# Optimization experiments

Hardware: AMD Instinct MI355X
Metric: run time of the kernel (lower is better)

## Reference

```python
import jax, jax.numpy as jnp
import numpy as np

EPS = 1e-12  # F.normalize default eps


def setup_inputs() -> dict:
    key = jax.random.key(0)
    k1, k2, k3, k4 = jax.random.split(key, 4)
    dim, heads = 192, 6
    B, H, W = 8, 128, 128
    x = jax.random.normal(k1, (B, dim, H, W), dtype=jnp.float32)
    qkv_w = jax.random.normal(k2, (3 * dim, dim), dtype=jnp.float32) * 0.05
    qkv_dw_w = jax.random.normal(k3, (3 * dim, 1, 3, 3), dtype=jnp.float32) * 0.05
    proj_w = jax.random.normal(k4, (dim, dim), dtype=jnp.float32) * 0.05
    temperature = jnp.ones((heads, 1, 1), dtype=jnp.float32)
    return {"x": x, "qkv_w": qkv_w, "qkv_dw_w": qkv_dw_w,
            "proj_w": proj_w, "temperature": temperature}


def _l2norm(t):
    # F.normalize(t, dim=-1): t / max(||t||_2, eps)
    n = jnp.sqrt(jnp.sum(t * t, axis=-1, keepdims=True))
    return t / jnp.maximum(n, EPS)


def reference(x, qkv_w, qkv_dw_w, proj_w, temperature):
    B, C, H, W = x.shape
    heads = temperature.shape[0]
    ch = C // heads  # channels per head

    # 1x1 pointwise conv (no bias)
    qkv = jnp.einsum('oc,bchw->bohw', qkv_w, x)
    # depthwise 3x3 conv, padding=1, groups = 3*C
    qkv = jax.lax.conv_general_dilated(
        qkv, qkv_dw_w, window_strides=(1, 1), padding='SAME',
        feature_group_count=3 * C,
        dimension_numbers=('NCHW', 'OIHW', 'NCHW'))

    q, k, v = jnp.split(qkv, 3, axis=1)
    # b (hd c) h w -> b hd c (h w)
    def split_heads(t):
        return t.reshape(B, heads, ch, H * W)
    q, k, v = split_heads(q), split_heads(k), split_heads(v)

    q = _l2norm(q)
    k = _l2norm(k)

    # channel attention: [b, hd, c, c], contraction over HW
    attn = jnp.einsum('bhcn,bhdn->bhcd', q, k) * temperature[None]
    attn = jax.nn.softmax(attn, axis=-1)

    out = jnp.einsum('bhcd,bhdn->bhcn', attn, v)  # [b, hd, c, HW]
    out = out.reshape(B, C, H, W)
    # final 1x1 projection
    return jnp.einsum('oc,bchw->bohw', proj_w, out)
```

## Files before the change

### kernel.cpp

```cpp
#include <hip/hip_runtime.h>
#include <type_traits>

typedef __attribute__((ext_vector_type(8))) short bf16x8;
typedef __attribute__((ext_vector_type(4))) float f32x4;

#define NB 8
#define NC 192
#define NO 576
#define NHW 16384
#define NH 6

__device__ __forceinline__ float bf2f(unsigned short u){
  return __uint_as_float(((unsigned int)u) << 16);
}
__device__ __forceinline__ unsigned short f2bf(float f){
  unsigned int u = __float_as_uint(f);
  u += 0x7FFFu + ((u >> 16) & 1u);
  return (unsigned short)(u >> 16);
}

__device__ __forceinline__ void st1(unsigned short* p, float v){ *p = f2bf(v); }
__device__ __forceinline__ void st1(float* p, float v){ *p = v; }

#define LSTR 200

__global__ void cvt_w(const float* __restrict__ w, unsigned short* __restrict__ wb, int n4){
  const int i = blockIdx.x*256 + threadIdx.x;
  if (i < n4){
    float4 f = *(const float4*)(w + (long long)i*4);
    *(ushort4*)(wb + (long long)i*4) = make_ushort4(f2bf(f.x), f2bf(f.y), f2bf(f.z), f2bf(f.w));
  }
}

template<typename BT, typename OT>
__global__ __launch_bounds__(256) void gemm192v2(
    const unsigned short* __restrict__ A, long long a_bstride, int o_tiles,
    const BT* __restrict__ Bm, long long b_bstride,
    OT* __restrict__ Out, long long o_bstride)
{
  __shared__ __align__(16) unsigned short Xt[128 * LSTR];
  const int t  = threadIdx.x;
  const int b  = blockIdx.z;
  const int n0 = blockIdx.x * 128;
  const BT* Bb = Bm + b_bstride * b;

  for (int idx = t; idx < 1536; idx += 256){
    const int n4 = (idx & 31) * 4;
    const int c  = (idx >> 5) * 4;
    if constexpr (std::is_same<BT, float>::value){
      float4 f0 = *(const float4*)(Bb + (long long)(c+0)*NHW + n0 + n4);
      float4 f1 = *(const float4*)(Bb + (long long)(c+1)*NHW + n0 + n4);
      float4 f2 = *(const float4*)(Bb + (long long)(c+2)*NHW + n0 + n4);
      float4 f3 = *(const float4*)(Bb + (long long)(c+3)*NHW + n0 + n4);
      *(ushort4*)&Xt[(n4+0)*LSTR + c] = make_ushort4(f2bf(f0.x), f2bf(f1.x), f2bf(f2.x), f2bf(f3.x));
      *(ushort4*)&Xt[(n4+1)*LSTR + c] = make_ushort4(f2bf(f0.y), f2bf(f1.y), f2bf(f2.y), f2bf(f3.y));
      *(ushort4*)&Xt[(n4+2)*LSTR + c] = make_ushort4(f2bf(f0.z), f2bf(f1.z), f2bf(f2.z), f2bf(f3.z));
      *(ushort4*)&Xt[(n4+3)*LSTR + c] = make_ushort4(f2bf(f0.w), f2bf(f1.w), f2bf(f2.w), f2bf(f3.w));
    } else {
      ushort4 u0 = *(const ushort4*)(Bb + (long long)(c+0)*NHW + n0 + n4);
      ushort4 u1 = *(const ushort4*)(Bb + (long long)(c+1)*NHW + n0 + n4);
      ushort4 u2 = *(const ushort4*)(Bb + (long long)(c+2)*NHW + n0 + n4);
      ushort4 u3 = *(const ushort4*)(Bb + (long long)(c+3)*NHW + n0 + n4);
      *(ushort4*)&Xt[(n4+0)*LSTR + c] = make_ushort4(u0.x, u1.x, u2.x, u3.x);
      *(ushort4*)&Xt[(n4+1)*LSTR + c] = make_ushort4(u0.y, u1.y, u2.y, u3.y);
      *(ushort4*)&Xt[(n4+2)*LSTR + c] = make_ushort4(u0.z, u1.z, u2.z, u3.z);
      *(ushort4*)&Xt[(n4+3)*LSTR + c] = make_ushort4(u0.w, u1.w, u2.w, u3.w);
    }
  }
  __syncthreads();

  const int l  = t & 63;
  const int w  = t >> 6;
  const int wo = (w >> 1) * 32;
  const int wn = (w & 1) * 64;
  const int lr = l & 15;
  const int lg = l >> 4;

  const unsigned short* Ab = A + a_bstride * b;
  OT* ob = Out + o_bstride * b;

  for (int ot = 0; ot < o_tiles; ++ot){
    const int o0 = ot * 64;
    const unsigned short* Aw = Ab + (long long)(o0 + wo + lr) * NC;

    f32x4 acc[2][4];
    #pragma unroll
    for (int i=0;i<2;i++)
      #pragma unroll
      for (int j=0;j<4;j++) acc[i][j] = (f32x4){0.f,0.f,0.f,0.f};

    #pragma unroll
    for (int k = 0; k < 192; k += 32){
      const int kc = k + lg*8;
      bf16x8 a0 = *(const bf16x8*)(Aw + kc);
      bf16x8 a1 = *(const bf16x8*)(Aw + 16*NC + kc);
      bf16x8 b0 = *(const bf16x8*)&Xt[(wn +      lr)*LSTR + kc];
      bf16x8 b1 = *(const bf16x8*)&Xt[(wn + 16 + lr)*LSTR + kc];
      bf16x8 b2 = *(const bf16x8*)&Xt[(wn + 32 + lr)*LSTR + kc];
      bf16x8 b3 = *(const bf16x8*)&Xt[(wn + 48 + lr)*LSTR + kc];
      acc[0][0] = __builtin_amdgcn_mfma_f32_16x16x32_bf16(a0, b0, acc[0][0], 0,0,0);
      acc[0][1] = __builtin_amdgcn_mfma_f32_16x16x32_bf16(a0, b1, acc[0][1], 0,0,0);
      acc[0][2] = __builtin_amdgcn_mfma_f32_16x16x32_bf16(a0, b2, acc[0][2], 0,0,0);
      acc[0][3] = __builtin_amdgcn_mfma_f32_16x16x32_bf16(a0, b3, acc[0][3], 0,0,0);
      acc[1][0] = __builtin_amdgcn_mfma_f32_16x16x32_bf16(a1, b0, acc[1][0], 0,0,0);
      acc[1][1] = __builtin_amdgcn_mfma_f32_16x16x32_bf16(a1, b1, acc[1][1], 0,0,0);
      acc[1][2] = __builtin_amdgcn_mfma_f32_16x16x32_bf16(a1, b2, acc[1][2], 0,0,0);
      acc[1][3] = __builtin_amdgcn_mfma_f32_16x16x32_bf16(a1, b3, acc[1][3], 0,0,0);
    }

    #pragma unroll
    for (int i=0;i<2;i++)
      #pragma unroll
      for (int j=0;j<4;j++)
        #pragma unroll
        for (int r=0;r<4;r++){
          const int oo = o0 + wo + i*16 + lg*4 + r;
          const int nn = n0 + wn + j*16 + lr;
          st1(ob + (long long)oo*NHW + nn, acc[i][j][r]);
        }
  }
}

__global__ __launch_bounds__(256) void dwconv2(const unsigned short* __restrict__ pw,
    const float* __restrict__ wdw, unsigned short* __restrict__ outp,
    float* __restrict__ sumsq)
{
  const int ch = blockIdx.x;
  const int b  = blockIdx.y;
  const int t  = threadIdx.x;
  const int lane  = t & 63;
  const int strip = t & 15;
  const int y0    = (t >> 4) * 8;
  const int x0    = strip * 8;

  const long long choff = ((long long)b*NO + ch) << 14;
  const unsigned short* base = pw + choff;
  unsigned short* ob = outp + choff;

  float w[9];
  #pragma unroll
  for (int i=0;i<9;i++) w[i] = wdw[ch*9 + i];

  float a0[8], a1[8], a2[8];
  #pragma unroll
  for (int i=0;i<8;i++){ a0[i]=0.f; a1[i]=0.f; a2[i]=0.f; }
  float ss = 0.f;

  #pragma unroll
  for (int r = 0; r < 10; ++r){
    const int yy = y0 - 1 + r;
    float f[8];
    if (yy >= 0 && yy <= 127){
      uint4 u = *(const uint4*)(base + (yy << 7) + x0);
      f[0]=bf2f((unsigned short)(u.x&0xffff)); f[1]=bf2f((unsigned short)(u.x>>16));
      f[2]=bf2f((unsigned short)(u.y&0xffff)); f[3]=bf2f((unsigned short)(u.y>>16));
      f[4]=bf2f((unsigned short)(u.z&0xffff)); f[5]=bf2f((unsigned short)(u.z>>16));
      f[6]=bf2f((unsigned short)(u.w&0xffff)); f[7]=bf2f((unsigned short)(u.w>>16));
    } else {
      #pragma unroll
      for (int i=0;i<8;i++) f[i]=0.f;
    }
    float lf = __shfl(f[7], lane - 1, 64);
    float rf = __shfl(f[0], lane + 1, 64);
    if (strip == 0)  lf = 0.f;
    if (strip == 15) rf = 0.f;

    #pragma unroll
    for (int i=0;i<8;i++){
      const float hL = (i==0) ? lf : f[i-1];
      const float hC = f[i];
      const float hR = (i==7) ? rf : f[i+1];
      a0[i] += w[6]*hL + w[7]*hC + w[8]*hR;
      a1[i] += w[3]*hL + w[4]*hC + w[5]*hR;
      a2[i] += w[0]*hL + w[1]*hC + w[2]*hR;
    }

    if (r >= 2){
      const int yo = y0 + r - 2;
      uint4 o;
      o.x = (unsigned int)f2bf(a0[0]) | ((unsigned int)f2bf(a0[1]) << 16);
      o.y = (unsigned int)f2bf(a0[2]) | ((unsigned int)f2bf(a0[3]) << 16);
      o.z = (unsigned int)f2bf(a0[4]) | ((unsigned int)f2bf(a0[5]) << 16);
      o.w = (unsigned int)f2bf(a0[6]) | ((unsigned int)f2bf(a0[7]) << 16);
      *(uint4*)(ob + (yo << 7) + x0) = o;
      #pragma unroll
      for (int i=0;i<8;i++) ss += a0[i]*a0[i];
    }
    #pragma unroll
    for (int i=0;i<8;i++){ a0[i]=a1[i]; a1[i]=a2[i]; a2[i]=0.f; }
  }

  if (ch < 384){
    #pragma unroll
    for (int off=32; off; off>>=1) ss += __shfl_down(ss, off);
    if (lane == 0) atomicAdd(&sumsq[b*384 + ch], ss);
  }
}

__global__ __launch_bounds__(256) void qkdots(const unsigned short* __restrict__ dw,
                                              float* __restrict__ partial)
{
  const int bh = blockIdx.x, ns = blockIdx.y;
  const int b = bh / 6, h = bh - b*6;
  const int t = threadIdx.x, w = t >> 6, l = t & 63, lr = l & 15, lg = l >> 4;
  const unsigned short* qb = dw + ((long long)b*NO + h*32) * NHW;
  const unsigned short* kb = dw + ((long long)b*NO + 192 + h*32) * NHW;
  const int nb = ns*1024 + w*256;
  f32x4 acc00 = {0.f,0.f,0.f,0.f}, acc01 = {0.f,0.f,0.f,0.f};
  f32x4 acc10 = {0.f,0.f,0.f,0.f}, acc11 = {0.f,0.f,0.f,0.f};
  #pragma unroll
  for (int kk=0; kk<8; kk++){
    const int n = nb + kk*32 + lg*8;
    bf16x8 a0 = *(const bf16x8*)(qb + (long long)(     lr)*NHW + n);
    bf16x8 a1 = *(const bf16x8*)(qb + (long long)(16 + lr)*NHW + n);
    bf16x8 b0 = *(const bf16x8*)(kb + (long long)(     lr)*NHW + n);
    bf16x8 b1 = *(const bf16x8*)(kb + (long long)(16 + lr)*NHW + n);
    acc00 = __builtin_amdgcn_mfma_f32_16x16x32_bf16(a0, b0, acc00, 0,0,0);
    acc01 = __builtin_amdgcn_mfma_f32_16x16x32_bf16(a0, b1, acc01, 0,0,0);
    acc10 = __builtin_amdgcn_mfma_f32_16x16x32_bf16(a1, b0, acc10, 0,0,0);
    acc11 = __builtin_amdgcn_mfma_f32_16x16x32_bf16(a1, b1, acc11, 0,0,0);
  }
  __shared__ float pl[4][32][32];
  #pragma unroll
  for (int r=0;r<4;r++){
    pl[w][ 0 + lg*4 + r][ 0 + lr] = acc00[r];
    pl[w][ 0 + lg*4 + r][16 + lr] = acc01[r];
    pl[w][16 + lg*4 + r][ 0 + lr] = acc10[r];
    pl[w][16 + lg*4 + r][16 + lr] = acc11[r];
  }
  __syncthreads();
  for (int e=t; e<1024; e+=256){
    const int r = e >> 5, c = e & 31;
    partial[((long long)bh*16 + ns)*1024 + e] = pl[0][r][c] + pl[1][r][c] + pl[2][r][c] + pl[3][r][c];
  }
}

__global__ __launch_bounds__(256) void softmaxk(const float* __restrict__ partial,
    const float* __restrict__ sumsq, const float* __restrict__ temp,
    float* __restrict__ attn)
{
  const int bh = blockIdx.x, b = bh / 6, h = bh - b*6;
  const int t = threadIdx.x;
  __shared__ float L[32][33];
  for (int e=t; e<1024; e+=256){
    const int c = e >> 5, d = e & 31;
    float s = 0.f;
    #pragma unroll
    for (int i=0;i<16;i++) s += partial[((long long)bh*16 + i)*1024 + e];
    const float nq = fmaxf(sqrtf(sumsq[b*384 + h*32 + c]),        1e-12f);
    const float nk = fmaxf(sqrtf(sumsq[b*384 + 192 + h*32 + d]),  1e-12f);
    L[c][d] = s / (nq * nk) * temp[h];
  }
  __syncthreads();
  if (t < 32){
    float m = -1e30f;
    #pragma unroll
    for (int d=0; d<32; d++) m = fmaxf(m, L[t][d]);
    float e[32]; float sum = 0.f;
    #pragma unroll
    for (int d=0; d<32; d++){ e[d] = expf(L[t][d] - m); sum += e[d]; }
    const float inv = 1.f / sum;
    #pragma unroll
    for (int d=0; d<32; d++) attn[(long long)bh*1024 + t*32 + d] = e[d] * inv;
  }
}

__global__ void mcombk(const float* __restrict__ proj, const float* __restrict__ attn,
                       unsigned short* __restrict__ mc)
{
  const int b = blockIdx.x, o = blockIdx.y, d = threadIdx.x;
  const int h = d >> 5, d32 = d & 31;
  const float* pr = proj + o*NC + h*32;
  const float* at = attn + ((long long)(b*NH + h))*1024 + d32;
  float acc = 0.f;
  #pragma unroll
  for (int c=0;c<32;c++) acc += pr[c] * at[c*32];
  mc[((long long)b*NC + o)*NC + d] = f2bf(acc);
}

extern "C" void kernel_launch(void* const* d_in, const int* in_sizes, int n_in,
                              void* d_out, int out_size, void* d_ws, size_t ws_size,
                              hipStream_t stream) {
  const float* x         = (const float*)d_in[0];
  const float* qkv_w     = (const float*)d_in[1];
  const float* qkv_dw_w  = (const float*)d_in[2];
  const float* proj_w    = (const float*)d_in[3];
  const float* temp      = (const float*)d_in[4];
  float* out = (float*)d_out;

  char* ws = (char*)d_ws;
  const size_t off_pw = 0;
  const size_t off_dw = (size_t)NB*NO*NHW*2;
  const size_t off_ss = off_dw + (size_t)NB*NO*NHW*2;
  const size_t off_pp = off_ss + (size_t)NB*384*4;
  const size_t off_at = off_pp + (size_t)48*16*1024*4;
  const size_t off_mc = off_at + (size_t)48*1024*4;
  const size_t off_wb = off_mc + (size_t)NB*NC*NC*2;

  unsigned short* pw     = (unsigned short*)(ws + off_pw);
  unsigned short* dwp    = (unsigned short*)(ws + off_dw);
  float*          sumsq  = (float*)(ws + off_ss);
  float*          partial= (float*)(ws + off_pp);
  float*          attn   = (float*)(ws + off_at);
  unsigned short* mcomb  = (unsigned short*)(ws + off_mc);
  unsigned short* wb     = (unsigned short*)(ws + off_wb);

  hipMemsetAsync(sumsq, 0, (size_t)NB*384*sizeof(float), stream);

  cvt_w<<<dim3((NO*NC/4 + 255)/256), 256, 0, stream>>>(qkv_w, wb, NO*NC/4);

  gemm192v2<float, unsigned short><<<dim3(128,1,NB), 256, 0, stream>>>(
      wb, 0LL, 9, x, (long long)NC*NHW, pw, (long long)NO*NHW);

  dwconv2<<<dim3(NO, NB), 256, 0, stream>>>(pw, qkv_dw_w, dwp, sumsq);

  qkdots<<<dim3(48,16), 256, 0, stream>>>(dwp, partial);

  softmaxk<<<48, 256, 0, stream>>>(partial, sumsq, temp, attn);

  mcombk<<<dim3(NB,192), 192, 0, stream>>>(proj_w, attn, mcomb);

  gemm192v2<unsigned short, float><<<dim3(128,1,NB), 256, 0, stream>>>(
      mcomb, (long long)NC*NC, 3, dwp + (long long)384*NHW, (long long)NO*NHW,
      out, (long long)NC*NHW);
}
```

Baseline: 363.3 us.

## Restructure 1x1-conv GEMM: 64-pixel tiles, register-held weights, vectorized stores

The pointwise GEMM kernel now processes 64 pixels per block instead of 128, doubling the grid. Each wave keeps its 16-row weight slice in registers across K and swaps MFMA operand roles so the pixel dimension is contiguous per lane. Outputs are written as packed 4-element vector stores instead of scalar strided stores. The cost is scalar (non-vector) global loads when staging the input tile and less reuse of each staged tile per block.

```diff
diff --git a/kernel.cpp b/kernel.cpp
--- a/kernel.cpp
+++ b/kernel.cpp
@@ -19,11 +19,6 @@
   return (unsigned short)(u >> 16);
 }
 
-__device__ __forceinline__ void st1(unsigned short* p, float v){ *p = f2bf(v); }
-__device__ __forceinline__ void st1(float* p, float v){ *p = v; }
-
-#define LSTR 200
-
 __global__ void cvt_w(const float* __restrict__ w, unsigned short* __restrict__ wb, int n4){
   const int i = blockIdx.x*256 + threadIdx.x;
   if (i < n4){
@@ -33,91 +28,83 @@
 }
 
 template<typename BT, typename OT>
-__global__ __launch_bounds__(256) void gemm192v2(
-    const unsigned short* __restrict__ A, long long a_bstride, int o_tiles,
+__global__ __launch_bounds__(256) void gemm192v3(
+    const unsigned short* __restrict__ W, long long w_bstride, int o_tiles,
     const BT* __restrict__ Bm, long long b_bstride,
     OT* __restrict__ Out, long long o_bstride)
 {
-  __shared__ __align__(16) unsigned short Xt[128 * LSTR];
+  __shared__ __align__(16) unsigned short Xt[64 * 200];
   const int t  = threadIdx.x;
   const int b  = blockIdx.z;
-  const int n0 = blockIdx.x * 128;
+  const int n0 = blockIdx.x * 64;
   const BT* Bb = Bm + b_bstride * b;
 
-  for (int idx = t; idx < 1536; idx += 256){
-    const int n4 = (idx & 31) * 4;
-    const int c  = (idx >> 5) * 4;
-    if constexpr (std::is_same<BT, float>::value){
-      float4 f0 = *(const float4*)(Bb + (long long)(c+0)*NHW + n0 + n4);
-      float4 f1 = *(const float4*)(Bb + (long long)(c+1)*NHW + n0 + n4);
-      float4 f2 = *(const float4*)(Bb + (long long)(c+2)*NHW + n0 + n4);
-      float4 f3 = *(const float4*)(Bb + (long long)(c+3)*NHW + n0 + n4);
-      *(ushort4*)&Xt[(n4+0)*LSTR + c] = make_ushort4(f2bf(f0.x), f2bf(f1.x), f2bf(f2.x), f2bf(f3.x));
-      *(ushort4*)&Xt[(n4+1)*LSTR + c] = make_ushort4(f2bf(f0.y), f2bf(f1.y), f2bf(f2.y), f2bf(f3.y));
-      *(ushort4*)&Xt[(n4+2)*LSTR + c] = make_ushort4(f2bf(f0.z), f2bf(f1.z), f2bf(f2.z), f2bf(f3.z));
-      *(ushort4*)&Xt[(n4+3)*LSTR + c] = make_ushort4(f2bf(f0.w), f2bf(f1.w), f2bf(f2.w), f2bf(f3.w));
-    } else {
-      ushort4 u0 = *(const ushort4*)(Bb + (long long)(c+0)*NHW + n0 + n4);
-      ushort4 u1 = *(const ushort4*)(Bb + (long long)(c+1)*NHW + n0 + n4);
-      ushort4 u2 = *(const ushort4*)(Bb + (long long)(c+2)*NHW + n0 + n4);
-      ushort4 u3 = *(const ushort4*)(Bb + (long long)(c+3)*NHW + n0 + n4);
-      *(ushort4*)&Xt[(n4+0)*LSTR + c] = make_ushort4(u0.x, u1.x, u2.x, u3.x);
-      *(ushort4*)&Xt[(n4+1)*LSTR + c] = make_ushort4(u0.y, u1.y, u2.y, u3.y);
-      *(ushort4*)&Xt[(n4+2)*LSTR + c] = make_ushort4(u0.z, u1.z, u2.z, u3.z);
-      *(ushort4*)&Xt[(n4+3)*LSTR + c] = make_ushort4(u0.w, u1.w, u2.w, u3.w);
+  {
+    const int n  = t & 63;
+    const int cb = (t >> 6) * 48;
+    #pragma unroll
+    for (int j = 0; j < 12; ++j){
+      const int c = cb + j*4;
+      unsigned short u0,u1,u2,u3;
+      if constexpr (std::is_same<BT,float>::value){
+        u0 = f2bf(Bb[(long long)(c+0)*NHW + n0 + n]);
+        u1 = f2bf(Bb[(long long)(c+1)*NHW + n0 + n]);
+        u2 = f2bf(Bb[(long long)(c+2)*NHW + n0 + n]);
+        u3 = f2bf(Bb[(long long)(c+3)*NHW + n0 + n]);
+      } else {
+        u0 = Bb[(long long)(c+0)*NHW + n0 + n];
+        u1 = Bb[(long long)(c+1)*NHW + n0 + n];
+        u2 = Bb[(long long)(c+2)*NHW + n0 + n];
+        u3 = Bb[(long long)(c+3)*NHW + n0 + n];
+      }
+      *(ushort4*)&Xt[n*200 + c] = make_ushort4(u0,u1,u2,u3);
     }
   }
   __syncthreads();
 
   const int l  = t & 63;
   const int w  = t >> 6;
-  const int wo = (w >> 1) * 32;
-  const int wn = (w & 1) * 64;
   const int lr = l & 15;
   const int lg = l >> 4;
 
-  const unsigned short* Ab = A + a_bstride * b;
+  const unsigned short* Wb = W + w_bstride * b;
   OT* ob = Out + o_bstride * b;
 
   for (int ot = 0; ot < o_tiles; ++ot){
-    const int o0 = ot * 64;
-    const unsigned short* Aw = Ab + (long long)(o0 + wo + lr) * NC;
-
-    f32x4 acc[2][4];
-    #pragma unroll
-    for (int i=0;i<2;i++)
+    const int obase = ot*64 + w*16;
+    const unsigned short* Wr = Wb + (long long)(obase + lr) * NC + lg*8;
+
+    bf16x8 Bf[6];
+    #pragma unroll
+    for (int kk = 0; kk < 6; ++kk) Bf[kk] = *(const bf16x8*)(Wr + kk*32);
+
+    f32x4 acc[4];
+    #pragma unroll
+    for (int i = 0; i < 4; ++i) acc[i] = (f32x4){0.f,0.f,0.f,0.f};
+
+    #pragma unroll
+    for (int kk = 0; kk < 6; ++kk){
+      const int kc = kk*32 + lg*8;
       #pragma unroll
-      for (int j=0;j<4;j++) acc[i][j] = (f32x4){0.f,0.f,0.f,0.f};
-
-    #pragma unroll
-    for (int k = 0; k < 192; k += 32){
-      const int kc = k + lg*8;
-      bf16x8 a0 = *(const bf16x8*)(Aw + kc);
-      bf16x8 a1 = *(const bf16x8*)(Aw + 16*NC + kc);
-      bf16x8 b0 = *(const bf16x8*)&Xt[(wn +      lr)*LSTR + kc];
-      bf16x8 b1 = *(const bf16x8*)&Xt[(wn + 16 + lr)*LSTR + kc];
-      bf16x8 b2 = *(const bf16x8*)&Xt[(wn + 32 + lr)*LSTR + kc];
-      bf16x8 b3 = *(const bf16x8*)&Xt[(wn + 48 + lr)*LSTR + kc];
-      acc[0][0] = __builtin_amdgcn_mfma_f32_16x16x32_bf16(a0, b0, acc[0][0], 0,0,0);
-      acc[0][1] = __builtin_amdgcn_mfma_f32_16x16x32_bf16(a0, b1, acc[0][1], 0,0,0);
-      acc[0][2] = __builtin_amdgcn_mfma_f32_16x16x32_bf16(a0, b2, acc[0][2], 0,0,0);
-      acc[0][3] = __builtin_amdgcn_mfma_f32_16x16x32_bf16(a0, b3, acc[0][3], 0,0,0);
-      acc[1][0] = __builtin_amdgcn_mfma_f32_16x16x32_bf16(a1, b0, acc[1][0], 0,0,0);
-      acc[1][1] = __builtin_amdgcn_mfma_f32_16x16x32_bf16(a1, b1, acc[1][1], 0,0,0);
-      acc[1][2] = __builtin_amdgcn_mfma_f32_16x16x32_bf16(a1, b2, acc[1][2], 0,0,0);
-      acc[1][3] = __builtin_amdgcn_mfma_f32_16x16x32_bf16(a1, b3, acc[1][3], 0,0,0);
-    }
-
-    #pragma unroll
-    for (int i=0;i<2;i++)
-      #pragma unroll
-      for (int j=0;j<4;j++)
-        #pragma unroll
-        for (int r=0;r<4;r++){
-          const int oo = o0 + wo + i*16 + lg*4 + r;
-          const int nn = n0 + wn + j*16 + lr;
-          st1(ob + (long long)oo*NHW + nn, acc[i][j][r]);
-        }
+      for (int i = 0; i < 4; ++i){
+        bf16x8 a = *(const bf16x8*)&Xt[(i*16 + lr)*200 + kc];
+        acc[i] = __builtin_amdgcn_mfma_f32_16x16x32_bf16(a, Bf[kk], acc[i], 0,0,0);
+      }
+    }
+
+    const long long o = obase + lr;
+    #pragma unroll
+    for (int i = 0; i < 4; ++i){
+      const int n = n0 + i*16 + lg*4;
+      if constexpr (std::is_same<OT, unsigned short>::value){
+        uint2 p;
+        p.x = (unsigned int)f2bf(acc[i][0]) | ((unsigned int)f2bf(acc[i][1]) << 16);
+        p.y = (unsigned int)f2bf(acc[i][2]) | ((unsigned int)f2bf(acc[i][3]) << 16);
+        *(uint2*)(ob + o*NHW + n) = p;
+      } else {
+        *(float4*)(ob + o*NHW + n) = make_float4(acc[i][0], acc[i][1], acc[i][2], acc[i][3]);
+      }
+    }
   }
 }
 
@@ -309,7 +296,7 @@
 
   cvt_w<<<dim3((NO*NC/4 + 255)/256), 256, 0, stream>>>(qkv_w, wb, NO*NC/4);
 
-  gemm192v2<float, unsigned short><<<dim3(128,1,NB), 256, 0, stream>>>(
+  gemm192v3<float, unsigned short><<<dim3(256,1,NB), 256, 0, stream>>>(
       wb, 0LL, 9, x, (long long)NC*NHW, pw, (long long)NO*NHW);
 
   dwconv2<<<dim3(NO, NB), 256, 0, stream>>>(pw, qkv_dw_w, dwp, sumsq);
@@ -320,7 +307,7 @@
 
   mcombk<<<dim3(NB,192), 192, 0, stream>>>(proj_w, attn, mcomb);
 
-  gemm192v2<unsigned short, float><<<dim3(128,1,NB), 256, 0, stream>>>(
+  gemm192v3<unsigned short, float><<<dim3(256,1,NB), 256, 0, stream>>>(
       mcomb, (long long)NC*NC, 3, dwp + (long long)384*NHW, (long long)NO*NHW,
       out, (long long)NC*NHW);
 }
```

Result: slower. 373.5 us (+2.8%).
